# Kernel tuning notes

Hardware: AMD Instinct MI355X
Metric: run time of the kernel (lower is better)

## Reference

```python
import jax, jax.numpy as jnp
import numpy as np

WS = 7            # window_size (attention is over 7x7x1 windows)
DIM = 128
DIM_HEAD = 32
HEADS = DIM // DIM_HEAD
SCALE = DIM_HEAD ** -0.5


def _rel_pos_indices(ws):
    # matches torch: 2D meshgrid over window_size, flattened, pairwise diffs
    pos = np.arange(ws)
    gi, gj = np.meshgrid(pos, pos, indexing='ij')
    grid = np.stack([gi.reshape(-1), gj.reshape(-1)], axis=-1)          # (ws^2, 2)
    rel = grid[:, None, :] - grid[None, :, :] + (ws - 1)                # (ws^2, ws^2, 2)
    idx = rel[..., 0] * (2 * ws - 1) + rel[..., 1]                      # (ws^2, ws^2)
    return jnp.asarray(idx, dtype=jnp.int32)


def setup_inputs() -> dict:
    key = jax.random.key(0)
    k1, k2, k3, k4 = jax.random.split(key, 4)
    x = jax.random.normal(k1, (4, 16, 16, 8, WS, WS, 1, DIM), dtype=jnp.float32)
    w_qkv = jax.random.normal(k2, (DIM, 3 * DIM), dtype=jnp.float32) * 0.02
    w_out = jax.random.normal(k3, (DIM, DIM), dtype=jnp.float32) * 0.02
    bias_table = jax.random.normal(k4, ((2 * WS - 1) ** 2, HEADS), dtype=jnp.float32) * 0.02
    return {"x": x, "w_qkv": w_qkv, "w_out": w_out, "bias_table": bias_table}


def reference(x, w_qkv, w_out, bias_table):
    b, X, Y, Z, w1, w2, w3, d = x.shape
    h, dh = HEADS, DIM_HEAD
    n = w1 * w2 * w3                                  # 49 tokens per window
    B = b * X * Y * Z                                 # fused window batch
    xf = x.reshape(B, n, d)
    qkv = xf @ w_qkv                                  # (B, n, 3d), no bias
    q, k, v = jnp.split(qkv, 3, axis=-1)

    def to_heads(t):
        return t.reshape(B, n, h, dh).transpose(0, 2, 1, 3)   # (B, h, n, dh)

    q = to_heads(q) * SCALE
    k = to_heads(k)
    v = to_heads(v)

    sim = jnp.einsum('bhid,bhjd->bhij', q, k)          # (B, h, n, n)
    bias = bias_table[_rel_pos_indices(WS)]            # (n, n, h) gather
    sim = sim + bias.transpose(2, 0, 1)                # broadcast over B
    attn = jax.nn.softmax(sim, axis=-1)                # dropout p=0.0
    out = jnp.einsum('bhij,bhjd->bhid', attn, v)       # (B, h, n, dh)
    out = out.transpose(0, 2, 1, 3).reshape(B, w1, w2, w3, d)
    out = out @ w_out                                  # (B, w1, w2, w3, d)
    return out.reshape(b, X, Y, Z, w1, w2, w3, d)
```

## Files before the change

### kernel.cpp

```cpp
#include <hip/hip_runtime.h>


typedef __bf16 bf16x8 __attribute__((ext_vector_type(8)));
typedef float f32x4 __attribute__((ext_vector_type(4)));
typedef unsigned short u16x8 __attribute__((ext_vector_type(8)));
typedef unsigned short u16x4 __attribute__((ext_vector_type(4)));

__device__ __forceinline__ unsigned short bf16c(float f) {
  return __builtin_bit_cast(unsigned short, (__bf16)f);
}
__device__ __forceinline__ bf16x8 ld8(const unsigned short* p) {
  return __builtin_bit_cast(bf16x8, *(const u16x8*)p);
}

#define XSb 0
#define Qb  6272
#define Kb  12544
#define VTb 0
#define Pb  6656
#define OSb 6656

__global__ void prep(const float* __restrict__ wq, const float* __restrict__ wo,
                     const float* __restrict__ bt,
                     unsigned short* __restrict__ wTq,
                     unsigned short* __restrict__ wTo,
                     float* __restrict__ bias2) {
  int t = blockIdx.x * 256 + threadIdx.x;
  if (t < 49152) {
    int n = t >> 7, k = t & 127;
    float v = wq[k * 384 + n];
    if (n < 128) v *= 0.17677669529663689f;
    wTq[t] = bf16c(v);
  } else if (t < 65536) {
    int i = t - 49152;
    int n = i >> 7, k = i & 127;
    wTo[i] = bf16c(wo[k * 128 + n]);
  } else {
    int i = t - 65536;
    int nt = i & 3, c = (i >> 2) & 15, ii = (i >> 6) & 63, hh = i >> 12;
    int j = nt * 16 + c;
    float v = -1e30f;
    if (j < 49) {
      int iq = ii < 49 ? ii : 48;
      int ri = iq / 7 - j / 7 + 6;
      int rj = iq % 7 - j % 7 + 6;
      v = bt[(ri * 13 + rj) * 4 + hh];
    }
    bias2[i] = v;
  }
}

__global__ __launch_bounds__(256, 4) void attn_fused(
    const float* __restrict__ x,
    const unsigned short* __restrict__ wTq,
    const unsigned short* __restrict__ wTo,
    const float4* __restrict__ bias2,
    float* __restrict__ out) {
  __shared__ __align__(16) unsigned short lds[18816];

  const int tid = threadIdx.x;
  const int wave = tid >> 6;
  const int lane = tid & 63;
  const int c16 = lane & 15;
  const int quad = lane >> 4;
  const int q4 = quad * 4;
  const int h = wave;
  const int MOFF[4] = {0, 16, 32, 33};

  const float* xb = x + (size_t)blockIdx.x * 6272;
  const f32x4 zero4 = {0.f, 0.f, 0.f, 0.f};

  for (int c = tid; c < 784; c += 256) {
    int row = c >> 4, c8 = c & 15;
    const float4* p = (const float4*)(xb + row * 128 + c8 * 8);
    float4 f0 = p[0], f1 = p[1];
    bf16x8 v;
    v[0] = (__bf16)f0.x; v[1] = (__bf16)f0.y; v[2] = (__bf16)f0.z; v[3] = (__bf16)f0.w;
    v[4] = (__bf16)f1.x; v[5] = (__bf16)f1.y; v[6] = (__bf16)f1.z; v[7] = (__bf16)f1.w;
    *(u16x8*)&lds[XSb + row * 128 + ((c8 ^ (row & 7)) << 3)] =
        __builtin_bit_cast(u16x8, v);
  }
  __syncthreads();

  const u16x8* wq8 = (const u16x8*)wTq;
  f32x4 vacc[4][2];
#pragma unroll
  for (int p = 0; p < 3; ++p) {
    f32x4 acc[4][2];
#pragma unroll
    for (int m = 0; m < 4; ++m) { acc[m][0] = zero4; acc[m][1] = zero4; }
#pragma unroll
    for (int kk = 0; kk < 4; ++kk) {
      bf16x8 a[4];
#pragma unroll
      for (int m = 0; m < 4; ++m) {
        int row = MOFF[m] + c16;
        a[m] = ld8(&lds[XSb + row * 128 + ((((kk << 2) | quad) ^ (row & 7)) << 3)]);
      }
      bf16x8 b[2];
#pragma unroll
      for (int j = 0; j < 2; ++j) {
        int n = (p * 8 + 2 * h + j) * 16 + c16;
        b[j] = __builtin_bit_cast(bf16x8, wq8[n * 16 + (kk << 2) + quad]);
      }
#pragma unroll
      for (int j = 0; j < 2; ++j)
#pragma unroll
        for (int m = 0; m < 4; ++m)
          acc[m][j] = __builtin_amdgcn_mfma_f32_16x16x32_bf16(a[m], b[j], acc[m][j], 0, 0, 0);
    }
    if (p < 2) {
      int base = (p == 0 ? Qb : Kb) + h * 1568;
#pragma unroll
      for (int m = 0; m < 4; ++m)
#pragma unroll
        for (int j = 0; j < 2; ++j)
#pragma unroll
          for (int r = 0; r < 4; ++r)
            lds[base + (MOFF[m] + q4 + r) * 32 + j * 16 + c16] = bf16c(acc[m][j][r]);
    } else {
#pragma unroll
      for (int m = 0; m < 4; ++m) { vacc[m][0] = acc[m][0]; vacc[m][1] = acc[m][1]; }
    }
  }

  bf16x8 aq[4];
#pragma unroll
  for (int m = 0; m < 4; ++m)
    aq[m] = ld8(&lds[Qb + h * 1568 + (MOFF[m] + c16) * 32 + quad * 8]);
  bf16x8 bk[4];
#pragma unroll
  for (int nt = 0; nt < 3; ++nt)
    bk[nt] = ld8(&lds[Kb + h * 1568 + (nt * 16 + c16) * 32 + quad * 8]);
  {
    bf16x8 z;
#pragma unroll
    for (int e = 0; e < 8; ++e) z[e] = (__bf16)0.f;
    bk[3] = z;
    if (c16 == 0) bk[3] = ld8(&lds[Kb + h * 1568 + 48 * 32 + quad * 8]);
  }
  __syncthreads();

  {
    int dh = lane & 31;
    lds[VTb + h * 1664 + dh * 52 + 49 + (lane >> 5)] = 0;
    if (lane < 32) lds[VTb + h * 1664 + dh * 52 + 51] = 0;
  }
#pragma unroll
  for (int m = 0; m < 4; ++m)
#pragma unroll
    for (int j = 0; j < 2; ++j)
#pragma unroll
      for (int r = 0; r < 4; ++r)
        lds[VTb + h * 1664 + (j * 16 + c16) * 52 + MOFF[m] + q4 + r] = bf16c(vacc[m][j][r]);

  float rinv[4][4];
#pragma unroll
  for (int m = 0; m < 4; ++m) {
    f32x4 s[4];
#pragma unroll
    for (int nt = 0; nt < 4; ++nt)
      s[nt] = __builtin_amdgcn_mfma_f32_16x16x32_bf16(aq[m], bk[nt], zero4, 0, 0, 0);
    float4 b4[4];
#pragma unroll
    for (int r = 0; r < 4; ++r)
      b4[r] = bias2[h * 1024 + (MOFF[m] + q4 + r) * 16 + c16];
#pragma unroll
    for (int r = 0; r < 4; ++r) {
      int row = MOFF[m] + q4 + r;
      float e0 = __expf(s[0][r] + b4[r].x);
      float e1 = __expf(s[1][r] + b4[r].y);
      float e2 = __expf(s[2][r] + b4[r].z);
      float e3 = __expf(s[3][r] + b4[r].w);
      float rs = (e0 + e1) + (e2 + e3);
      rs += __shfl_xor(rs, 1);
      rs += __shfl_xor(rs, 2);
      rs += __shfl_xor(rs, 4);
      rs += __shfl_xor(rs, 8);
      rinv[m][r] = __builtin_amdgcn_rcpf(rs);
      unsigned short* pr = &lds[Pb + h * 2548 + row * 52 + c16];
      pr[0] = bf16c(e0);
      pr[16] = bf16c(e1);
      pr[32] = bf16c(e2);
      if (c16 < 4) pr[48] = bf16c(e3);
    }
  }

  bf16x8 pa[2][4];
#pragma unroll
  for (int kk = 0; kk < 2; ++kk)
#pragma unroll
    for (int m = 0; m < 4; ++m) {
      const unsigned short* pp = &lds[Pb + h * 2548 + (MOFF[m] + c16) * 52 + kk * 32 + quad * 8];
      u16x4 lo = *(const u16x4*)pp;
      u16x4 hi = *(const u16x4*)(pp + 4);
      if (kk == 1) {
        if (quad >= 2) hi = (u16x4)0;
        if (quad == 3) lo = (u16x4)0;
      }
      pa[kk][m] = __builtin_bit_cast(bf16x8,
                  __builtin_shufflevector(lo, hi, 0, 1, 2, 3, 4, 5, 6, 7));
    }
  bf16x8 bv[2][2];
#pragma unroll
  for (int kk = 0; kk < 2; ++kk)
#pragma unroll
    for (int j = 0; j < 2; ++j) {
      const unsigned short* vp = &lds[VTb + h * 1664 + (j * 16 + c16) * 52 + kk * 32 + quad * 8];
      u16x4 lo = *(const u16x4*)vp;
      u16x4 hi = *(const u16x4*)(vp + 4);
      if (kk == 1) {
        if (quad >= 2) hi = (u16x4)0;
        if (quad == 3) lo = (u16x4)0;
      }
      bv[kk][j] = __builtin_bit_cast(bf16x8,
                  __builtin_shufflevector(lo, hi, 0, 1, 2, 3, 4, 5, 6, 7));
    }
  __syncthreads();

  f32x4 o[4][2];
#pragma unroll
  for (int m = 0; m < 4; ++m) { o[m][0] = zero4; o[m][1] = zero4; }
#pragma unroll
  for (int kk = 0; kk < 2; ++kk)
#pragma unroll
    for (int j = 0; j < 2; ++j)
#pragma unroll
      for (int m = 0; m < 4; ++m)
        o[m][j] = __builtin_amdgcn_mfma_f32_16x16x32_bf16(pa[kk][m], bv[kk][j], o[m][j], 0, 0, 0);

#pragma unroll
  for (int m = 0; m < 4; ++m)
#pragma unroll
    for (int j = 0; j < 2; ++j)
#pragma unroll
      for (int r = 0; r < 4; ++r)
        lds[OSb + (MOFF[m] + q4 + r) * 136 + h * 32 + j * 16 + c16] =
            bf16c(o[m][j][r] * rinv[m][r]);
  __syncthreads();

  const u16x8* wo8 = (const u16x8*)wTo;
  f32x4 oc[4][2];
#pragma unroll
  for (int m = 0; m < 4; ++m) { oc[m][0] = zero4; oc[m][1] = zero4; }
#pragma unroll
  for (int kk = 0; kk < 4; ++kk) {
    bf16x8 a2[4];
#pragma unroll
    for (int m = 0; m < 4; ++m)
      a2[m] = ld8(&lds[OSb + (MOFF[m] + c16) * 136 + kk * 32 + quad * 8]);
#pragma unroll
    for (int j = 0; j < 2; ++j) {
      int n = (2 * wave + j) * 16 + c16;
      bf16x8 b2 = __builtin_bit_cast(bf16x8, wo8[n * 16 + (kk << 2) + quad]);
#pragma unroll
      for (int m = 0; m < 4; ++m)
        oc[m][j] = __builtin_amdgcn_mfma_f32_16x16x32_bf16(a2[m], b2, oc[m][j], 0, 0, 0);
    }
  }

  float* op = out + (size_t)blockIdx.x * 6272;
#pragma unroll
  for (int m = 0; m < 4; ++m)
#pragma unroll
    for (int r = 0; r < 4; ++r) {
      int row = MOFF[m] + q4 + r;
#pragma unroll
      for (int j = 0; j < 2; ++j)
        op[row * 128 + (2 * wave + j) * 16 + c16] = oc[m][j][r];
    }
}

extern "C" void kernel_launch(void* const* d_in, const int* in_sizes, int n_in,
                              void* d_out, int out_size, void* d_ws, size_t ws_size,
                              hipStream_t stream) {
  const float* x = (const float*)d_in[0];
  const float* wq = (const float*)d_in[1];
  const float* wo = (const float*)d_in[2];
  const float* bt = (const float*)d_in[3];

  unsigned short* wTq = (unsigned short*)d_ws;
  unsigned short* wTo = wTq + 49152;
  float* bias2 = (float*)((char*)d_ws + 131072);

  prep<<<320, 256, 0, stream>>>(wq, wo, bt, wTq, wTo, bias2);
  attn_fused<<<8192, 256, 0, stream>>>(x, wTq, wTo, (const float4*)bias2, (float*)d_out);
}
```

Baseline: 454.2 us.

## Keep Q/K/V and softmax probabilities in registers via transposed MFMA layouts

Reorders the QKV projection MFMAs (swapping operands for Q and K) so their accumulator layouts can be repacked directly into bf16 MFMA operands for QK^T and PV. This removes the LDS round trips for Q, K, V^T and P. The bias is folded into the QK^T accumulator init with a re-laid-out bias table. Softmax normalization is now applied before PV, and the row sum needs only two cross-lane shuffles. LDS shrinks from about 37KB to 16KB, which may raise occupancy; the cost is more register pressure and padded rows (zero-filled x rows 49-63).

```diff
diff --git a/kernel.cpp b/kernel.cpp
--- a/kernel.cpp
+++ b/kernel.cpp
@@ -4,7 +4,6 @@
 typedef __bf16 bf16x8 __attribute__((ext_vector_type(8)));
 typedef float f32x4 __attribute__((ext_vector_type(4)));
 typedef unsigned short u16x8 __attribute__((ext_vector_type(8)));
-typedef unsigned short u16x4 __attribute__((ext_vector_type(4)));
 
 __device__ __forceinline__ unsigned short bf16c(float f) {
   return __builtin_bit_cast(unsigned short, (__bf16)f);
@@ -12,13 +11,6 @@
 __device__ __forceinline__ bf16x8 ld8(const unsigned short* p) {
   return __builtin_bit_cast(bf16x8, *(const u16x8*)p);
 }
-
-#define XSb 0
-#define Qb  6272
-#define Kb  12544
-#define VTb 0
-#define Pb  6656
-#define OSb 6656
 
 __global__ void prep(const float* __restrict__ wq, const float* __restrict__ wo,
                      const float* __restrict__ bt,
@@ -37,14 +29,16 @@
     wTo[i] = bf16c(wo[k * 128 + n]);
   } else {
     int i = t - 65536;
-    int nt = i & 3, c = (i >> 2) & 15, ii = (i >> 6) & 63, hh = i >> 12;
-    int j = nt * 16 + c;
+    int r = i & 3, q = (i >> 2) & 3, jt = (i >> 4) & 3;
+    int c = (i >> 6) & 15, it = (i >> 10) & 3, h = (i >> 12) & 3;
+    int j = jt * 16 + q * 4 + r;
+    int ii = it * 16 + c;
+    int iq = ii < 49 ? ii : 48;
     float v = -1e30f;
     if (j < 49) {
-      int iq = ii < 49 ? ii : 48;
       int ri = iq / 7 - j / 7 + 6;
       int rj = iq % 7 - j % 7 + 6;
-      v = bt[(ri * 13 + rj) * 4 + hh];
+      v = bt[(ri * 13 + rj) * 4 + h];
     }
     bias2[i] = v;
   }
@@ -54,9 +48,9 @@
     const float* __restrict__ x,
     const unsigned short* __restrict__ wTq,
     const unsigned short* __restrict__ wTo,
-    const float4* __restrict__ bias2,
+    const f32x4* __restrict__ bias2,
     float* __restrict__ out) {
-  __shared__ __align__(16) unsigned short lds[18816];
+  __shared__ __align__(16) unsigned short lds[8192];
 
   const int tid = threadIdx.x;
   const int wave = tid >> 6;
@@ -65,25 +59,30 @@
   const int quad = lane >> 4;
   const int q4 = quad * 4;
   const int h = wave;
-  const int MOFF[4] = {0, 16, 32, 33};
+  const f32x4 zero4 = {0.f, 0.f, 0.f, 0.f};
 
   const float* xb = x + (size_t)blockIdx.x * 6272;
-  const f32x4 zero4 = {0.f, 0.f, 0.f, 0.f};
-
-  for (int c = tid; c < 784; c += 256) {
+
+  for (int c = tid; c < 1024; c += 256) {
     int row = c >> 4, c8 = c & 15;
-    const float4* p = (const float4*)(xb + row * 128 + c8 * 8);
-    float4 f0 = p[0], f1 = p[1];
     bf16x8 v;
-    v[0] = (__bf16)f0.x; v[1] = (__bf16)f0.y; v[2] = (__bf16)f0.z; v[3] = (__bf16)f0.w;
-    v[4] = (__bf16)f1.x; v[5] = (__bf16)f1.y; v[6] = (__bf16)f1.z; v[7] = (__bf16)f1.w;
-    *(u16x8*)&lds[XSb + row * 128 + ((c8 ^ (row & 7)) << 3)] =
-        __builtin_bit_cast(u16x8, v);
+    if (row < 49) {
+      const float4* p = (const float4*)(xb + row * 128 + c8 * 8);
+      float4 f0 = p[0], f1 = p[1];
+      v[0] = (__bf16)f0.x; v[1] = (__bf16)f0.y; v[2] = (__bf16)f0.z; v[3] = (__bf16)f0.w;
+      v[4] = (__bf16)f1.x; v[5] = (__bf16)f1.y; v[6] = (__bf16)f1.z; v[7] = (__bf16)f1.w;
+    } else {
+#pragma unroll
+      for (int e = 0; e < 8; ++e) v[e] = (__bf16)0.f;
+    }
+    *(u16x8*)&lds[row * 128 + ((c8 ^ (row & 7)) << 3)] = __builtin_bit_cast(u16x8, v);
   }
   __syncthreads();
 
   const u16x8* wq8 = (const u16x8*)wTq;
-  f32x4 vacc[4][2];
+  bf16x8 bq[4];
+  bf16x8 ak[4];
+  bf16x8 bv[2][2];
 #pragma unroll
   for (int p = 0; p < 3; ++p) {
     f32x4 acc[4][2];
@@ -93,153 +92,91 @@
     for (int kk = 0; kk < 4; ++kk) {
       bf16x8 a[4];
 #pragma unroll
-      for (int m = 0; m < 4; ++m) {
-        int row = MOFF[m] + c16;
-        a[m] = ld8(&lds[XSb + row * 128 + ((((kk << 2) | quad) ^ (row & 7)) << 3)]);
+      for (int m = 0; m < 4; ++m)
+        a[m] = ld8(&lds[(16 * m + c16) * 128 + ((((kk << 2) | quad) ^ (c16 & 7)) << 3)]);
+      bf16x8 b[2];
+#pragma unroll
+      for (int j = 0; j < 2; ++j)
+        b[j] = __builtin_bit_cast(bf16x8,
+               wq8[(p * 128 + h * 32 + j * 16 + c16) * 16 + (kk << 2) + quad]);
+#pragma unroll
+      for (int j = 0; j < 2; ++j)
+#pragma unroll
+        for (int m = 0; m < 4; ++m)
+          acc[m][j] = (p < 2)
+            ? __builtin_amdgcn_mfma_f32_16x16x32_bf16(b[j], a[m], acc[m][j], 0, 0, 0)
+            : __builtin_amdgcn_mfma_f32_16x16x32_bf16(a[m], b[j], acc[m][j], 0, 0, 0);
+    }
+    if (p == 0) {
+#pragma unroll
+      for (int it = 0; it < 4; ++it)
+#pragma unroll
+        for (int e = 0; e < 8; ++e)
+          bq[it][e] = (__bf16)acc[it][e >> 2][e & 3];
+    } else if (p == 1) {
+#pragma unroll
+      for (int jt = 0; jt < 4; ++jt)
+#pragma unroll
+        for (int e = 0; e < 8; ++e)
+          ak[jt][e] = (__bf16)acc[jt][e >> 2][e & 3];
+    } else {
+#pragma unroll
+      for (int kk = 0; kk < 2; ++kk)
+#pragma unroll
+        for (int j2 = 0; j2 < 2; ++j2)
+#pragma unroll
+          for (int e = 0; e < 8; ++e)
+            bv[kk][j2][e] = (__bf16)acc[2 * kk + (e >> 2)][j2][e & 3];
+    }
+  }
+  __syncthreads();
+
+#pragma unroll
+  for (int it = 0; it < 4; ++it) {
+    f32x4 s[4];
+#pragma unroll
+    for (int jt = 0; jt < 4; ++jt) {
+      f32x4 b4 = bias2[((h * 4 + it) * 16 + c16) * 16 + jt * 4 + quad];
+      s[jt] = __builtin_amdgcn_mfma_f32_16x16x32_bf16(ak[jt], bq[it], b4, 0, 0, 0);
+    }
+    float e[4][4];
+#pragma unroll
+    for (int jt = 0; jt < 4; ++jt)
+#pragma unroll
+      for (int r = 0; r < 4; ++r)
+        e[jt][r] = __expf(s[jt][r]);
+    float rs = ((e[0][0] + e[0][1]) + (e[0][2] + e[0][3]))
+             + ((e[1][0] + e[1][1]) + (e[1][2] + e[1][3]))
+             + ((e[2][0] + e[2][1]) + (e[2][2] + e[2][3]))
+             + ((e[3][0] + e[3][1]) + (e[3][2] + e[3][3]));
+    rs += __shfl_xor(rs, 16);
+    rs += __shfl_xor(rs, 32);
+    float rinv = __builtin_amdgcn_rcpf(rs);
+    bf16x8 pa[2];
+#pragma unroll
+    for (int kk = 0; kk < 2; ++kk)
+#pragma unroll
+      for (int ee = 0; ee < 8; ++ee)
+        pa[kk][ee] = (__bf16)(e[2 * kk + (ee >> 2)][ee & 3] * rinv);
+    f32x4 o0 = zero4, o1 = zero4;
+#pragma unroll
+    for (int kk = 0; kk < 2; ++kk) {
+      o0 = __builtin_amdgcn_mfma_f32_16x16x32_bf16(pa[kk], bv[kk][0], o0, 0, 0, 0);
+      o1 = __builtin_amdgcn_mfma_f32_16x16x32_bf16(pa[kk], bv[kk][1], o1, 0, 0, 0);
+    }
+#pragma unroll
+    for (int r = 0; r < 4; ++r) {
+      int row = 16 * it + q4 + r;
+      if (row < 49) {
+        lds[row * 136 + h * 32 + c16]      = bf16c(o0[r]);
+        lds[row * 136 + h * 32 + 16 + c16] = bf16c(o1[r]);
       }
-      bf16x8 b[2];
-#pragma unroll
-      for (int j = 0; j < 2; ++j) {
-        int n = (p * 8 + 2 * h + j) * 16 + c16;
-        b[j] = __builtin_bit_cast(bf16x8, wq8[n * 16 + (kk << 2) + quad]);
-      }
-#pragma unroll
-      for (int j = 0; j < 2; ++j)
-#pragma unroll
-        for (int m = 0; m < 4; ++m)
-          acc[m][j] = __builtin_amdgcn_mfma_f32_16x16x32_bf16(a[m], b[j], acc[m][j], 0, 0, 0);
-    }
-    if (p < 2) {
-      int base = (p == 0 ? Qb : Kb) + h * 1568;
-#pragma unroll
-      for (int m = 0; m < 4; ++m)
-#pragma unroll
-        for (int j = 0; j < 2; ++j)
-#pragma unroll
-          for (int r = 0; r < 4; ++r)
-            lds[base + (MOFF[m] + q4 + r) * 32 + j * 16 + c16] = bf16c(acc[m][j][r]);
-    } else {
-#pragma unroll
-      for (int m = 0; m < 4; ++m) { vacc[m][0] = acc[m][0]; vacc[m][1] = acc[m][1]; }
-    }
-  }
-
-  bf16x8 aq[4];
-#pragma unroll
-  for (int m = 0; m < 4; ++m)
-    aq[m] = ld8(&lds[Qb + h * 1568 + (MOFF[m] + c16) * 32 + quad * 8]);
-  bf16x8 bk[4];
-#pragma unroll
-  for (int nt = 0; nt < 3; ++nt)
-    bk[nt] = ld8(&lds[Kb + h * 1568 + (nt * 16 + c16) * 32 + quad * 8]);
-  {
-    bf16x8 z;
-#pragma unroll
-    for (int e = 0; e < 8; ++e) z[e] = (__bf16)0.f;
-    bk[3] = z;
-    if (c16 == 0) bk[3] = ld8(&lds[Kb + h * 1568 + 48 * 32 + quad * 8]);
+    }
   }
   __syncthreads();
 
-  {
-    int dh = lane & 31;
-    lds[VTb + h * 1664 + dh * 52 + 49 + (lane >> 5)] = 0;
-    if (lane < 32) lds[VTb + h * 1664 + dh * 52 + 51] = 0;
-  }
-#pragma unroll
-  for (int m = 0; m < 4; ++m)
-#pragma unroll
-    for (int j = 0; j < 2; ++j)
-#pragma unroll
-      for (int r = 0; r < 4; ++r)
-        lds[VTb + h * 1664 + (j * 16 + c16) * 52 + MOFF[m] + q4 + r] = bf16c(vacc[m][j][r]);
-
-  float rinv[4][4];
-#pragma unroll
-  for (int m = 0; m < 4; ++m) {
-    f32x4 s[4];
-#pragma unroll
-    for (int nt = 0; nt < 4; ++nt)
-      s[nt] = __builtin_amdgcn_mfma_f32_16x16x32_bf16(aq[m], bk[nt], zero4, 0, 0, 0);
-    float4 b4[4];
-#pragma unroll
-    for (int r = 0; r < 4; ++r)
-      b4[r] = bias2[h * 1024 + (MOFF[m] + q4 + r) * 16 + c16];
-#pragma unroll
-    for (int r = 0; r < 4; ++r) {
-      int row = MOFF[m] + q4 + r;
-      float e0 = __expf(s[0][r] + b4[r].x);
-      float e1 = __expf(s[1][r] + b4[r].y);
-      float e2 = __expf(s[2][r] + b4[r].z);
-      float e3 = __expf(s[3][r] + b4[r].w);
-      float rs = (e0 + e1) + (e2 + e3);
-      rs += __shfl_xor(rs, 1);
-      rs += __shfl_xor(rs, 2);
-      rs += __shfl_xor(rs, 4);
-      rs += __shfl_xor(rs, 8);
-      rinv[m][r] = __builtin_amdgcn_rcpf(rs);
-      unsigned short* pr = &lds[Pb + h * 2548 + row * 52 + c16];
-      pr[0] = bf16c(e0);
-      pr[16] = bf16c(e1);
-      pr[32] = bf16c(e2);
-      if (c16 < 4) pr[48] = bf16c(e3);
-    }
-  }
-
-  bf16x8 pa[2][4];
-#pragma unroll
-  for (int kk = 0; kk < 2; ++kk)
-#pragma unroll
-    for (int m = 0; m < 4; ++m) {
-      const unsigned short* pp = &lds[Pb + h * 2548 + (MOFF[m] + c16) * 52 + kk * 32 + quad * 8];
-      u16x4 lo = *(const u16x4*)pp;
-      u16x4 hi = *(const u16x4*)(pp + 4);
-      if (kk == 1) {
-        if (quad >= 2) hi = (u16x4)0;
-        if (quad == 3) lo = (u16x4)0;
-      }
-      pa[kk][m] = __builtin_bit_cast(bf16x8,
-                  __builtin_shufflevector(lo, hi, 0, 1, 2, 3, 4, 5, 6, 7));
-    }
-  bf16x8 bv[2][2];
-#pragma unroll
-  for (int kk = 0; kk < 2; ++kk)
-#pragma unroll
-    for (int j = 0; j < 2; ++j) {
-      const unsigned short* vp = &lds[VTb + h * 1664 + (j * 16 + c16) * 52 + kk * 32 + quad * 8];
-      u16x4 lo = *(const u16x4*)vp;
-      u16x4 hi = *(const u16x4*)(vp + 4);
-      if (kk == 1) {
-        if (quad >= 2) hi = (u16x4)0;
-        if (quad == 3) lo = (u16x4)0;
-      }
-      bv[kk][j] = __builtin_bit_cast(bf16x8,
-                  __builtin_shufflevector(lo, hi, 0, 1, 2, 3, 4, 5, 6, 7));
-    }
-  __syncthreads();
-
-  f32x4 o[4][2];
-#pragma unroll
-  for (int m = 0; m < 4; ++m) { o[m][0] = zero4; o[m][1] = zero4; }
-#pragma unroll
-  for (int kk = 0; kk < 2; ++kk)
-#pragma unroll
-    for (int j = 0; j < 2; ++j)
-#pragma unroll
-      for (int m = 0; m < 4; ++m)
-        o[m][j] = __builtin_amdgcn_mfma_f32_16x16x32_bf16(pa[kk][m], bv[kk][j], o[m][j], 0, 0, 0);
-
-#pragma unroll
-  for (int m = 0; m < 4; ++m)
-#pragma unroll
-    for (int j = 0; j < 2; ++j)
-#pragma unroll
-      for (int r = 0; r < 4; ++r)
-        lds[OSb + (MOFF[m] + q4 + r) * 136 + h * 32 + j * 16 + c16] =
-            bf16c(o[m][j][r] * rinv[m][r]);
-  __syncthreads();
-
   const u16x8* wo8 = (const u16x8*)wTo;
+  const int MOFF2[4] = {0, 16, 32, 33};
   f32x4 oc[4][2];
 #pragma unroll
   for (int m = 0; m < 4; ++m) { oc[m][0] = zero4; oc[m][1] = zero4; }
@@ -248,11 +185,11 @@
     bf16x8 a2[4];
 #pragma unroll
     for (int m = 0; m < 4; ++m)
-      a2[m] = ld8(&lds[OSb + (MOFF[m] + c16) * 136 + kk * 32 + quad * 8]);
+      a2[m] = ld8(&lds[(MOFF2[m] + c16) * 136 + kk * 32 + quad * 8]);
 #pragma unroll
     for (int j = 0; j < 2; ++j) {
-      int n = (2 * wave + j) * 16 + c16;
-      bf16x8 b2 = __builtin_bit_cast(bf16x8, wo8[n * 16 + (kk << 2) + quad]);
+      bf16x8 b2 = __builtin_bit_cast(bf16x8,
+                  wo8[((2 * wave + j) * 16 + c16) * 16 + (kk << 2) + quad]);
 #pragma unroll
       for (int m = 0; m < 4; ++m)
         oc[m][j] = __builtin_amdgcn_mfma_f32_16x16x32_bf16(a2[m], b2, oc[m][j], 0, 0, 0);
@@ -264,7 +201,7 @@
   for (int m = 0; m < 4; ++m)
 #pragma unroll
     for (int r = 0; r < 4; ++r) {
-      int row = MOFF[m] + q4 + r;
+      int row = MOFF2[m] + q4 + r;
 #pragma unroll
       for (int j = 0; j < 2; ++j)
         op[row * 128 + (2 * wave + j) * 16 + c16] = oc[m][j][r];
@@ -284,5 +221,5 @@
   float* bias2 = (float*)((char*)d_ws + 131072);
 
   prep<<<320, 256, 0, stream>>>(wq, wo, bt, wTq, wTo, bias2);
-  attn_fused<<<8192, 256, 0, stream>>>(x, wTq, wTo, (const float4*)bias2, (float*)d_out);
-}
+  attn_fused<<<8192, 256, 0, stream>>>(x, wTq, wTo, (const f32x4*)bias2, (float*)d_out);
+}
```

Result: slower. 514.6 us (+13.3%).
